# Performance work log

Hardware: AMD Instinct MI355X
Metric: run time of the kernel (lower is better)

The kernel has to match this reference:

```python
import jax, jax.numpy as jnp
import numpy as np

B, N, D, H = 2, 64, 256, 8
DK = D // H
EPS = 1e-5


def layer_norm(x, g, b):
    mu = jnp.mean(x, axis=-1, keepdims=True)
    var = jnp.var(x, axis=-1, keepdims=True)
    return (x - mu) * jax.lax.rsqrt(var + EPS) * g + b


def setup_inputs() -> dict:
    key = jax.random.key(0)
    ks = jax.random.split(key, 12)
    s = 1.0 / np.sqrt(D)
    inp = {
        "x": jax.random.normal(ks[0], (B, N, N, D), jnp.float32),
        "W_lk": jax.random.uniform(ks[1], (D, D), jnp.float32, -s, s),
        "W_rk": jax.random.uniform(ks[2], (D, D), jnp.float32, -s, s),
        "W_lv": jax.random.uniform(ks[3], (D, D), jnp.float32, -s, s),
        "W_rv": jax.random.uniform(ks[4], (D, D), jnp.float32, -s, s),
        "W_out": jax.random.uniform(ks[5], (D, D), jnp.float32, -s, s),
        "ln_agg_g": jnp.ones((D,), jnp.float32),
        "ln_agg_b": jnp.zeros((D,), jnp.float32),
        "W1": jax.random.uniform(ks[6], (D, 2 * D), jnp.float32, -s, s),
        "b1": jnp.zeros((2 * D,), jnp.float32),
        "W2": jax.random.uniform(ks[7], (2 * D, D), jnp.float32, -1.0 / np.sqrt(2 * D), 1.0 / np.sqrt(2 * D)),
        "b2": jnp.zeros((D,), jnp.float32),
        "ln2_g": jnp.ones((D,), jnp.float32),
        "ln2_b": jnp.zeros((D,), jnp.float32),
    }
    return inp


def reference(x, W_lk, W_rk, W_lv, W_rv, W_out, ln_agg_g, ln_agg_b, W1, b1, W2, b2, ln2_g, ln2_b):
    b, n = x.shape[0], x.shape[1]
    # projections (no bias), split into heads: [b, n, n, H, DK]
    lk = (x @ W_lk).reshape(b, n, n, H, DK)
    rk = (x @ W_rk).reshape(b, n, n, H, DK)
    lv = (x @ W_lv).reshape(b, n, n, H, DK)
    rv = (x @ W_rv).reshape(b, n, n, H, DK)
    # triangle attention scores over intermediate node 'a'
    scores = jnp.einsum('bxahd,bayhd->bxayh', lk, rk) / np.sqrt(DK)
    att = jax.nn.softmax(scores, axis=2)
    # fused triangle value aggregation: sum_a att * lv[x,a] * rv[a,y]
    o = jnp.einsum('bxayh,bxahd,bayhd->bxyhd', att, lv, rv)
    o = o.reshape(b, n, n, D) @ W_out
    # FFN block (dropout = 0)
    h = layer_norm(x + o, ln_agg_g, ln_agg_b)
    m = jax.nn.relu(h @ W1 + b1) @ W2 + b2
    return layer_norm(m + h, ln2_g, ln2_b)
```

## Files before the change

kernel.cpp:

```cpp
#include <hip/hip_runtime.h>

#define ROWS 8192
#define DIM  256

typedef short short8 __attribute__((ext_vector_type(8)));
typedef float f4     __attribute__((ext_vector_type(4)));

__device__ __forceinline__ float bf2f(unsigned int u16) {
    union { unsigned int i; float f; } v;
    v.i = (u16 & 0xffffu) << 16;
    return v.f;
}
__device__ __forceinline__ unsigned short f2bf(float f) {
    union { float f; unsigned int u; } v; v.f = f;
    unsigned int r = v.u + 0x7fffu + ((v.u >> 16) & 1u);
    return (unsigned short)(r >> 16);
}

__global__ __launch_bounds__(256)
void cast_all(const float* __restrict__ x, unsigned short* __restrict__ xb,
              const float* __restrict__ w0, const float* __restrict__ w1,
              const float* __restrict__ w2, const float* __restrict__ w3,
              const float* __restrict__ w4, const float* __restrict__ w5,
              const float* __restrict__ w6, unsigned short* __restrict__ wt)
{
    if (blockIdx.x < 2048) {
        const size_t i = ((size_t)blockIdx.x * 256 + threadIdx.x) * 4;
        float4 v = *(const float4*)(x + i);
        uint2 p;
        p.x = f2bf(v.x) | ((unsigned int)f2bf(v.y) << 16);
        p.y = f2bf(v.z) | ((unsigned int)f2bf(v.w) << 16);
        *(uint2*)(xb + i) = p;
        return;
    }
    __shared__ float t[32][33];
    int id = blockIdx.x - 2048;
    const float* src; int K, N, Ntiles; size_t doff;
    if (id < 320) {
        int w = id >> 6; id &= 63; K = 256; N = 256; Ntiles = 8;
        doff = (size_t)w * 65536;
        src = (w == 0) ? w0 : (w == 1) ? w1 : (w == 2) ? w2 : (w == 3) ? w3 : w4;
    } else if (id < 448) {
        id -= 320; K = 256; N = 512; Ntiles = 16; doff = 327680; src = w5;
    } else {
        id -= 448; K = 512; N = 256; Ntiles = 8;  doff = 458752; src = w6;
    }
    const int tk = id / Ntiles, tn = id % Ntiles;
    const int k0 = tk * 32, n0 = tn * 32;
    const int c = threadIdx.x & 31, r8 = threadIdx.x >> 5;
    for (int rr = r8; rr < 32; rr += 8)
        t[rr][c] = src[(size_t)(k0 + rr) * N + n0 + c];
    __syncthreads();
    for (int rr = r8; rr < 32; rr += 8)
        wt[doff + (size_t)(n0 + rr) * K + k0 + c] = f2bf(t[c][rr]);
}

__global__ __launch_bounds__(1024, 1)
void proj_mfma(const unsigned short* __restrict__ A, const unsigned short* __restrict__ WT,
               unsigned short* __restrict__ projT)
{
    __shared__ unsigned short WL[256 * 256];
    const int lane = threadIdx.x & 63, wave = threadIdx.x >> 6;
    const int wsel = blockIdx.x;
    const int col0 = (wave >> 2) * 64;
    const int m0 = blockIdx.y * 128 + (wave & 3) * 32;
    const int lm = lane & 15, lk8 = (lane >> 4) * 8;
    const unsigned short* W = WT + (size_t)wsel * 65536;
    unsigned short* dst = projT + (size_t)wsel * 2097152;

    {
        const int tid = threadIdx.x;
        #pragma unroll
        for (int it = 0; it < 8; ++it) {
            const int c = tid + it * 1024;
            const int col = c >> 5, ch = c & 31;
            const uint4 v = *(const uint4*)(W + (size_t)col * 256 + ch * 8);
            *(uint4*)((char*)WL + col * 512 + ((ch ^ (col & 7)) << 4)) = v;
        }
    }
    __syncthreads();

    f4 acc[2][4];
    #pragma unroll
    for (int i = 0; i < 2; ++i)
        #pragma unroll
        for (int j = 0; j < 4; ++j) acc[i][j] = (f4){0.f, 0.f, 0.f, 0.f};

    #pragma unroll 2
    for (int kc = 0; kc < 256; kc += 32) {
        short8 af[2], bf[4];
        #pragma unroll
        for (int i = 0; i < 2; ++i)
            af[i] = *(const short8*)(A + (size_t)(m0 + i * 16 + lm) * 256 + kc + lk8);
        #pragma unroll
        for (int j = 0; j < 4; ++j) {
            const int cl = col0 + j * 16 + lm;
            const int kch = (kc + lk8) >> 3;
            bf[j] = *(const short8*)((char*)WL + cl * 512 + ((kch ^ (cl & 7)) << 4));
        }
        #pragma unroll
        for (int i = 0; i < 2; ++i)
            #pragma unroll
            for (int j = 0; j < 4; ++j)
                acc[i][j] = __builtin_amdgcn_mfma_f32_16x16x32_bf16(af[i], bf[j], acc[i][j], 0, 0, 0);
    }

    const int rbase = (lane >> 4) * 4;
    const int swap = (wsel == 3);
    #pragma unroll
    for (int i = 0; i < 2; ++i)
        #pragma unroll
        for (int j = 0; j < 4; ++j) {
            const int c = col0 + j * 16 + lm;
            const int h = c >> 5, d = c & 31;
            #pragma unroll
            for (int r = 0; r < 4; ++r) {
                const int m = m0 + i * 16 + rbase + r;
                const int b = m >> 12, ii = (m >> 6) & 63, jj = m & 63;
                const int p = swap ? jj : ii;
                const int q = swap ? ii : jj;
                const size_t idx = ((((size_t)b * 8 + h) * 64 + p) * 64 + q) * 32 + d;
                dst[idx] = f2bf(acc[i][j][r]);
            }
        }
}

__global__ __launch_bounds__(256)
void scores_mfma(const unsigned short* __restrict__ lkT, const unsigned short* __restrict__ rkT,
                 unsigned short* __restrict__ S)
{
    const int lane = threadIdx.x & 63, wave = threadIdx.x >> 6;
    const int bi = blockIdx.x;
    const int b = bi >> 7, h = (bi >> 4) & 7, a = (bi & 15) * 4 + wave;
    const size_t bh = (size_t)b * 8 + h;
    const int lm = lane & 15, lk8 = (lane >> 4) * 8;

    short8 af[4], bf[4];
    #pragma unroll
    for (int t = 0; t < 4; ++t) {
        af[t] = *(const short8*)(lkT + ((bh * 64 + (t * 16 + lm)) * 64 + a) * 32 + lk8);
        bf[t] = *(const short8*)(rkT + ((bh * 64 + a) * 64 + (t * 16 + lm)) * 32 + lk8);
    }
    const int rbase = (lane >> 4) * 4;
    unsigned short* Sb = S + bh * 262144 + a * 64;
    #pragma unroll
    for (int mt = 0; mt < 4; ++mt)
        #pragma unroll
        for (int nt = 0; nt < 4; ++nt) {
            f4 acc = (f4){0.f, 0.f, 0.f, 0.f};
            acc = __builtin_amdgcn_mfma_f32_16x16x32_bf16(af[mt], bf[nt], acc, 0, 0, 0);
            #pragma unroll
            for (int r = 0; r < 4; ++r) {
                const int xx = mt * 16 + rbase + r;
                const int yy = nt * 16 + lm;
                Sb[(size_t)xx * 4096 + yy] = f2bf(acc[r] * 0.17677669529663687f);
            }
        }
}

__global__ __launch_bounds__(256)
void softmax_agg(const unsigned short* __restrict__ S, const unsigned short* __restrict__ lvT,
                 const unsigned short* __restrict__ rvT, unsigned short* __restrict__ obuf)
{
    __shared__ float att[64][64];
    __shared__ float lvL[64][32];
    __shared__ float smx[4][64], ssm[4][64], invL[64];
    const int bi = blockIdx.x;
    const int b = bi >> 9, h = (bi >> 6) & 7, x = bi & 63;
    const size_t bh = (size_t)b * 8 + h;
    const int tid = threadIdx.x;

    {
        const int a = tid >> 2, yo = (tid & 3) * 16;
        const unsigned short* Sp = S + (bh * 64 + x) * 4096 + a * 64 + yo;
        uint4 p0 = *(const uint4*)(Sp);
        uint4 p1 = *(const uint4*)(Sp + 8);
        att[a][yo +  0] = bf2f(p0.x); att[a][yo +  1] = bf2f(p0.x >> 16);
        att[a][yo +  2] = bf2f(p0.y); att[a][yo +  3] = bf2f(p0.y >> 16);
        att[a][yo +  4] = bf2f(p0.z); att[a][yo +  5] = bf2f(p0.z >> 16);
        att[a][yo +  6] = bf2f(p0.w); att[a][yo +  7] = bf2f(p0.w >> 16);
        att[a][yo +  8] = bf2f(p1.x); att[a][yo +  9] = bf2f(p1.x >> 16);
        att[a][yo + 10] = bf2f(p1.y); att[a][yo + 11] = bf2f(p1.y >> 16);
        att[a][yo + 12] = bf2f(p1.z); att[a][yo + 13] = bf2f(p1.z >> 16);
        att[a][yo + 14] = bf2f(p1.w); att[a][yo + 15] = bf2f(p1.w >> 16);
        const int d0 = (tid & 3) * 8;
        uint4 q = *(const uint4*)(lvT + ((bh * 64 + x) * 64 + a) * 32 + d0);
        lvL[a][d0 + 0] = bf2f(q.x); lvL[a][d0 + 1] = bf2f(q.x >> 16);
        lvL[a][d0 + 2] = bf2f(q.y); lvL[a][d0 + 3] = bf2f(q.y >> 16);
        lvL[a][d0 + 4] = bf2f(q.z); lvL[a][d0 + 5] = bf2f(q.z >> 16);
        lvL[a][d0 + 6] = bf2f(q.w); lvL[a][d0 + 7] = bf2f(q.w >> 16);
    }
    __syncthreads();

    {
        const int y = tid & 63, az = tid >> 6;
        float mx = -1e30f;
        for (int a = az; a < 64; a += 4) mx = fmaxf(mx, att[a][y]);
        smx[az][y] = mx;
    }
    __syncthreads();

    {
        const int y = tid & 63, az = tid >> 6;
        const float mx = fmaxf(fmaxf(smx[0][y], smx[1][y]), fmaxf(smx[2][y], smx[3][y]));
        float s = 0.f;
        for (int a = az; a < 64; a += 4) {
            float e = __expf(att[a][y] - mx);
            att[a][y] = e;
            s += e;
        }
        ssm[az][y] = s;
    }
    __syncthreads();
    if (tid < 64)
        invL[tid] = 1.f / (ssm[0][tid] + ssm[1][tid] + ssm[2][tid] + ssm[3][tid]);
    __syncthreads();

    {
        const int dp = tid & 15, yb = tid >> 4;
        #pragma unroll
        for (int it = 0; it < 4; ++it) {
            const int y = yb + it * 16;
            const unsigned short* rvr = rvT + (bh * 64 + y) * 2048 + dp * 2;
            float a0 = 0.f, a1 = 0.f;
            #pragma unroll 8
            for (int a = 0; a < 64; ++a) {
                unsigned int pk = *(const unsigned int*)(rvr + a * 32);
                float w = att[a][y];
                a0 = fmaf(w * lvL[a][2 * dp],     bf2f(pk),       a0);
                a1 = fmaf(w * lvL[a][2 * dp + 1], bf2f(pk >> 16), a1);
            }
            const float inv = invL[y];
            a0 *= inv; a1 *= inv;
            unsigned int st = f2bf(a0) | ((unsigned int)f2bf(a1) << 16);
            *(unsigned int*)(obuf + (((size_t)b * 64 + x) * 64 + y) * 256 + h * 32 + dp * 2) = st;
        }
    }
}

__device__ __forceinline__ int swz8(int r, int c, int rl) {
    return r * rl + ((((c >> 3) ^ (r & 7)) << 3) | (c & 7));
}

__global__ __launch_bounds__(512, 2)
void ffn_fused(const unsigned short* __restrict__ A,
               const unsigned short* __restrict__ WoT,
               const unsigned short* __restrict__ W1T,
               const unsigned short* __restrict__ W2T,
               const float* __restrict__ xres,
               const float* __restrict__ g1, const float* __restrict__ be1,
               const float* __restrict__ b1, const float* __restrict__ b2,
               const float* __restrict__ g2, const float* __restrict__ be2,
               float* __restrict__ out)
{
    __shared__ unsigned short hs[32 * 256];
    __shared__ unsigned short ms[32 * 512];
    __shared__ float ps[32][8], pq[32][8];
    const int lane = threadIdx.x & 63, wave = threadIdx.x >> 6;
    const int m0 = blockIdx.x * 32;
    const int lm = lane & 15, lk8 = (lane >> 4) * 8;
    const int rbase = (lane >> 4) * 4;
    const int col0 = wave * 32;
    const int rot8  = (blockIdx.x >> 3) & 7;
    const int rot16 = (blockIdx.x >> 3) & 15;
    float hreg[2][2][4];

    {
        f4 acc[2][2];
        #pragma unroll
        for (int i = 0; i < 2; ++i)
            #pragma unroll
            for (int j = 0; j < 2; ++j) acc[i][j] = (f4){0.f, 0.f, 0.f, 0.f};
        #pragma unroll
        for (int t = 0; t < 8; ++t) {
            const int kc = ((t + rot8) & 7) * 32;
            short8 af[2], bf[2];
            #pragma unroll
            for (int i = 0; i < 2; ++i)
                af[i] = *(const short8*)(A + (size_t)(m0 + i * 16 + lm) * 256 + kc + lk8);
            #pragma unroll
            for (int j = 0; j < 2; ++j)
                bf[j] = *(const short8*)(WoT + (size_t)(col0 + j * 16 + lm) * 256 + kc + lk8);
            #pragma unroll
            for (int i = 0; i < 2; ++i)
                #pragma unroll
                for (int j = 0; j < 2; ++j)
                    acc[i][j] = __builtin_amdgcn_mfma_f32_16x16x32_bf16(af[i], bf[j], acc[i][j], 0, 0, 0);
        }
        float v[2][2][4], s[2][4], q[2][4];
        #pragma unroll
        for (int i = 0; i < 2; ++i)
            #pragma unroll
            for (int r = 0; r < 4; ++r) { s[i][r] = 0.f; q[i][r] = 0.f; }
        #pragma unroll
        for (int i = 0; i < 2; ++i)
            #pragma unroll
            for (int j = 0; j < 2; ++j) {
                const int n = col0 + j * 16 + lm;
                #pragma unroll
                for (int r = 0; r < 4; ++r) {
                    const float t = acc[i][j][r] + xres[(size_t)(m0 + i * 16 + rbase + r) * 256 + n];
                    v[i][j][r] = t;
                    s[i][r] += t;
                    q[i][r] = fmaf(t, t, q[i][r]);
                }
            }
        #pragma unroll
        for (int off = 1; off < 16; off <<= 1)
            #pragma unroll
            for (int i = 0; i < 2; ++i)
                #pragma unroll
                for (int r = 0; r < 4; ++r) {
                    s[i][r] += __shfl_xor(s[i][r], off);
                    q[i][r] += __shfl_xor(q[i][r], off);
                }
        if (lm == 0)
            #pragma unroll
            for (int i = 0; i < 2; ++i)
                #pragma unroll
                for (int r = 0; r < 4; ++r) {
                    ps[i * 16 + rbase + r][wave] = s[i][r];
                    pq[i * 16 + rbase + r][wave] = q[i][r];
                }
        __syncthreads();
        #pragma unroll
        for (int i = 0; i < 2; ++i)
            #pragma unroll
            for (int r = 0; r < 4; ++r) {
                const int lr = i * 16 + rbase + r;
                const float Sm = ps[lr][0] + ps[lr][1] + ps[lr][2] + ps[lr][3]
                               + ps[lr][4] + ps[lr][5] + ps[lr][6] + ps[lr][7];
                const float Qm = pq[lr][0] + pq[lr][1] + pq[lr][2] + pq[lr][3]
                               + pq[lr][4] + pq[lr][5] + pq[lr][6] + pq[lr][7];
                const float mu = Sm * (1.f / 256.f);
                const float ri = rsqrtf(Qm * (1.f / 256.f) - mu * mu + 1e-5f);
                #pragma unroll
                for (int j = 0; j < 2; ++j) {
                    const int n = col0 + j * 16 + lm;
                    const unsigned short hb16 = f2bf((v[i][j][r] - mu) * ri * g1[n] + be1[n]);
                    hs[swz8(lr, n, 256)] = hb16;
                    hreg[i][j][r] = bf2f(hb16);
                }
            }
    }
    __syncthreads();

    {
        const int c0 = wave * 64;
        f4 acc2[2][4];
        #pragma unroll
        for (int i = 0; i < 2; ++i)
            #pragma unroll
            for (int j = 0; j < 4; ++j) acc2[i][j] = (f4){0.f, 0.f, 0.f, 0.f};
        #pragma unroll
        for (int t = 0; t < 8; ++t) {
            const int kc = ((t + rot8) & 7) * 32;
            short8 af[2], bf[4];
            #pragma unroll
            for (int i = 0; i < 2; ++i)
                af[i] = *(const short8*)(hs + swz8(i * 16 + lm, kc + lk8, 256));
            #pragma unroll
            for (int j = 0; j < 4; ++j)
                bf[j] = *(const short8*)(W1T + (size_t)(c0 + j * 16 + lm) * 256 + kc + lk8);
            #pragma unroll
            for (int i = 0; i < 2; ++i)
                #pragma unroll
                for (int j = 0; j < 4; ++j)
                    acc2[i][j] = __builtin_amdgcn_mfma_f32_16x16x32_bf16(af[i], bf[j], acc2[i][j], 0, 0, 0);
        }
        #pragma unroll
        for (int i = 0; i < 2; ++i)
            #pragma unroll
            for (int j = 0; j < 4; ++j) {
                const int n = c0 + j * 16 + lm;
                const float bb = b1[n];
                #pragma unroll
                for (int r = 0; r < 4; ++r)
                    ms[swz8(i * 16 + rbase + r, n, 512)] = f2bf(fmaxf(acc2[i][j][r] + bb, 0.f));
            }
    }
    __syncthreads();

    {
        f4 acc[2][2];
        #pragma unroll
        for (int i = 0; i < 2; ++i)
            #pragma unroll
            for (int j = 0; j < 2; ++j) acc[i][j] = (f4){0.f, 0.f, 0.f, 0.f};
        #pragma unroll
        for (int t = 0; t < 16; ++t) {
            const int kc = ((t + rot16) & 15) * 32;
            short8 af[2], bf[2];
            #pragma unroll
            for (int i = 0; i < 2; ++i)
                af[i] = *(const short8*)(ms + swz8(i * 16 + lm, kc + lk8, 512));
            #pragma unroll
            for (int j = 0; j < 2; ++j)
                bf[j] = *(const short8*)(W2T + (size_t)(col0 + j * 16 + lm) * 512 + kc + lk8);
            #pragma unroll
            for (int i = 0; i < 2; ++i)
                #pragma unroll
                for (int j = 0; j < 2; ++j)
                    acc[i][j] = __builtin_amdgcn_mfma_f32_16x16x32_bf16(af[i], bf[j], acc[i][j], 0, 0, 0);
        }
        float v[2][2][4], s[2][4], q[2][4];
        #pragma unroll
        for (int i = 0; i < 2; ++i)
            #pragma unroll
            for (int r = 0; r < 4; ++r) { s[i][r] = 0.f; q[i][r] = 0.f; }
        #pragma unroll
        for (int i = 0; i < 2; ++i)
            #pragma unroll
            for (int j = 0; j < 2; ++j) {
                const int n = col0 + j * 16 + lm;
                const float bb = b2[n];
                #pragma unroll
                for (int r = 0; r < 4; ++r) {
                    const float t = acc[i][j][r] + bb + hreg[i][j][r];
                    v[i][j][r] = t;
                    s[i][r] += t;
                    q[i][r] = fmaf(t, t, q[i][r]);
                }
            }
        #pragma unroll
        for (int off = 1; off < 16; off <<= 1)
            #pragma unroll
            for (int i = 0; i < 2; ++i)
                #pragma unroll
                for (int r = 0; r < 4; ++r) {
                    s[i][r] += __shfl_xor(s[i][r], off);
                    q[i][r] += __shfl_xor(q[i][r], off);
                }
        if (lm == 0)
            #pragma unroll
            for (int i = 0; i < 2; ++i)
                #pragma unroll
                for (int r = 0; r < 4; ++r) {
                    ps[i * 16 + rbase + r][wave] = s[i][r];
                    pq[i * 16 + rbase + r][wave] = q[i][r];
                }
        __syncthreads();
        #pragma unroll
        for (int i = 0; i < 2; ++i)
            #pragma unroll
            for (int r = 0; r < 4; ++r) {
                const int lr = i * 16 + rbase + r;
                const float Sm = ps[lr][0] + ps[lr][1] + ps[lr][2] + ps[lr][3]
                               + ps[lr][4] + ps[lr][5] + ps[lr][6] + ps[lr][7];
                const float Qm = pq[lr][0] + pq[lr][1] + pq[lr][2] + pq[lr][3]
                               + pq[lr][4] + pq[lr][5] + pq[lr][6] + pq[lr][7];
                const float mu = Sm * (1.f / 256.f);
                const float ri = rsqrtf(Qm * (1.f / 256.f) - mu * mu + 1e-5f);
                const int m = m0 + lr;
                #pragma unroll
                for (int j = 0; j < 2; ++j) {
                    const int n = col0 + j * 16 + lm;
                    out[(size_t)m * 256 + n] = (v[i][j][r] - mu) * ri * g2[n] + be2[n];
                }
            }
    }
}

extern "C" void kernel_launch(void* const* d_in, const int* in_sizes, int n_in,
                              void* d_out, int out_size, void* d_ws, size_t ws_size,
                              hipStream_t stream)
{
    const float* x    = (const float*)d_in[0];
    const float* Wlk  = (const float*)d_in[1];
    const float* Wrk  = (const float*)d_in[2];
    const float* Wlv  = (const float*)d_in[3];
    const float* Wrv  = (const float*)d_in[4];
    const float* Wout = (const float*)d_in[5];
    const float* g1   = (const float*)d_in[6];
    const float* be1  = (const float*)d_in[7];
    const float* W1   = (const float*)d_in[8];
    const float* b1   = (const float*)d_in[9];
    const float* W2   = (const float*)d_in[10];
    const float* b2   = (const float*)d_in[11];
    const float* g2   = (const float*)d_in[12];
    const float* be2  = (const float*)d_in[13];

    char* base = (char*)d_ws;
    const size_t MB = 1ull << 20;
    unsigned short* xb    = (unsigned short*)(base + 0);
    unsigned short* obufb = (unsigned short*)(base + 0);
    unsigned short* projT = (unsigned short*)(base + 4 * MB);
    unsigned short* lkT   = projT;
    unsigned short* rkT   = projT + 2097152;
    unsigned short* lvT   = projT + 2 * 2097152;
    unsigned short* rvT   = projT + 3 * 2097152;
    unsigned short* Sbuf  = (unsigned short*)(base + 32 * MB);
    unsigned short* WT    = (unsigned short*)(base + 40 * MB);

    cast_all<<<2624, 256, 0, stream>>>(x, xb, Wlk, Wrk, Wlv, Wrv, Wout, W1, W2, WT);
    proj_mfma<<<dim3(4, 64), 1024, 0, stream>>>(xb, WT, projT);
    scores_mfma<<<256, 256, 0, stream>>>(lkT, rkT, Sbuf);
    softmax_agg<<<1024, 256, 0, stream>>>(Sbuf, lvT, rvT, obufb);
    ffn_fused<<<256, 512, 0, stream>>>(obufb, WT + 262144, WT + 327680, WT + 458752,
                                       x, g1, be1, b1, b2, g2, be2, (float*)d_out);
}
```

Before: 158.2 us.

## Stage FFN weights through double-buffered LDS via async global_load_lds

The fused FFN kernel now loads each K-slice of WoT, W1T and W2T into a double-buffered shared-memory buffer with global_load_lds, prefetching the next slice while MFMAs run on the current one. The A tile is also staged into LDS, and residual values are preloaded into registers. This replaces direct per-wave global loads of the weight fragments with shared, asynchronous staging. In exchange it adds about 80KB of LDS per block, which may reduce occupancy below the launch bound of 2 blocks, adds a barrier every K step, and removes the per-block K rotation.

```diff
diff --git a/kernel.cpp b/kernel.cpp
--- a/kernel.cpp
+++ b/kernel.cpp
@@ -16,6 +16,10 @@
     unsigned int r = v.u + 0x7fffu + ((v.u >> 16) & 1u);
     return (unsigned short)(r >> 16);
 }
+
+#define GLD(g, l) __builtin_amdgcn_global_load_lds( \
+    (const __attribute__((address_space(1))) void*)(g), \
+    (__attribute__((address_space(3))) void*)(l), 16, 0, 0)
 
 __global__ __launch_bounds__(256)
 void cast_all(const float* __restrict__ x, unsigned short* __restrict__ xb,
@@ -253,74 +257,109 @@
                const float* __restrict__ g2, const float* __restrict__ be2,
                float* __restrict__ out)
 {
+    __shared__ unsigned short As[32 * 256];
     __shared__ unsigned short hs[32 * 256];
     __shared__ unsigned short ms[32 * 512];
+    __shared__ unsigned short wbuf[2 * 16384];
     __shared__ float ps[32][8], pq[32][8];
     const int lane = threadIdx.x & 63, wave = threadIdx.x >> 6;
     const int m0 = blockIdx.x * 32;
     const int lm = lane & 15, lk8 = (lane >> 4) * 8;
-    const int rbase = (lane >> 4) * 4;
+    const int og = lane >> 4;
+    const int rbase = og * 4;
     const int col0 = wave * 32;
-    const int rot8  = (blockIdx.x >> 3) & 7;
-    const int rot16 = (blockIdx.x >> 3) & 15;
     float hreg[2][2][4];
 
+    float xr[2][2][4];
+    #pragma unroll
+    for (int i = 0; i < 2; ++i)
+        #pragma unroll
+        for (int j = 0; j < 2; ++j)
+            #pragma unroll
+            for (int r = 0; r < 4; ++r)
+                xr[i][j][r] = xres[(size_t)(m0 + i * 16 + rbase + r) * 256 + col0 + j * 16 + lm];
+
+    #pragma unroll
+    for (int s = 0; s < 2; ++s) {
+        const int idx = (wave * 2 + s) * 64 + lane;
+        GLD(A + (size_t)(m0 + (idx & 31)) * 256 + (idx >> 5) * 8, As + (wave * 2 + s) * 512);
+    }
+    #pragma unroll
+    for (int s = 0; s < 2; ++s) {
+        const int idx = (wave * 2 + s) * 64 + lane;
+        GLD(WoT + (size_t)(idx & 255) * 256 + (idx >> 8) * 8, wbuf + (wave * 2 + s) * 512);
+    }
+    __syncthreads();
+
     {
         f4 acc[2][2];
         #pragma unroll
         for (int i = 0; i < 2; ++i)
             #pragma unroll
             for (int j = 0; j < 2; ++j) acc[i][j] = (f4){0.f, 0.f, 0.f, 0.f};
-        #pragma unroll
         for (int t = 0; t < 8; ++t) {
-            const int kc = ((t + rot8) & 7) * 32;
+            if (t < 7) {
+                unsigned short* db = wbuf + ((t + 1) & 1) * 8192;
+                const int kcn = (t + 1) * 32;
+                #pragma unroll
+                for (int s = 0; s < 2; ++s) {
+                    const int idx = (wave * 2 + s) * 64 + lane;
+                    GLD(WoT + (size_t)(idx & 255) * 256 + kcn + (idx >> 8) * 8, db + (wave * 2 + s) * 512);
+                }
+            }
+            const unsigned short* wb = wbuf + (t & 1) * 8192;
+            const int oA = t * 4 + og;
             short8 af[2], bf[2];
             #pragma unroll
             for (int i = 0; i < 2; ++i)
-                af[i] = *(const short8*)(A + (size_t)(m0 + i * 16 + lm) * 256 + kc + lk8);
+                af[i] = *(const short8*)(As + (oA * 32 + i * 16 + lm) * 8);
             #pragma unroll
             for (int j = 0; j < 2; ++j)
-                bf[j] = *(const short8*)(WoT + (size_t)(col0 + j * 16 + lm) * 256 + kc + lk8);
+                bf[j] = *(const short8*)(wb + (og * 256 + col0 + j * 16 + lm) * 8);
             #pragma unroll
             for (int i = 0; i < 2; ++i)
                 #pragma unroll
                 for (int j = 0; j < 2; ++j)
                     acc[i][j] = __builtin_amdgcn_mfma_f32_16x16x32_bf16(af[i], bf[j], acc[i][j], 0, 0, 0);
-        }
-        float v[2][2][4], s[2][4], q[2][4];
-        #pragma unroll
-        for (int i = 0; i < 2; ++i)
-            #pragma unroll
-            for (int r = 0; r < 4; ++r) { s[i][r] = 0.f; q[i][r] = 0.f; }
-        #pragma unroll
-        for (int i = 0; i < 2; ++i)
-            #pragma unroll
-            for (int j = 0; j < 2; ++j) {
-                const int n = col0 + j * 16 + lm;
+            __syncthreads();
+        }
+        #pragma unroll
+        for (int s = 0; s < 4; ++s) {
+            const int idx = (wave * 4 + s) * 64 + lane;
+            GLD(W1T + (size_t)(idx & 511) * 256 + (idx >> 9) * 8, wbuf + (wave * 4 + s) * 512);
+        }
+        float v[2][2][4], s1[2][4], q1[2][4];
+        #pragma unroll
+        for (int i = 0; i < 2; ++i)
+            #pragma unroll
+            for (int r = 0; r < 4; ++r) { s1[i][r] = 0.f; q1[i][r] = 0.f; }
+        #pragma unroll
+        for (int i = 0; i < 2; ++i)
+            #pragma unroll
+            for (int j = 0; j < 2; ++j)
                 #pragma unroll
                 for (int r = 0; r < 4; ++r) {
-                    const float t = acc[i][j][r] + xres[(size_t)(m0 + i * 16 + rbase + r) * 256 + n];
+                    const float t = acc[i][j][r] + xr[i][j][r];
                     v[i][j][r] = t;
-                    s[i][r] += t;
-                    q[i][r] = fmaf(t, t, q[i][r]);
-                }
-            }
+                    s1[i][r] += t;
+                    q1[i][r] = fmaf(t, t, q1[i][r]);
+                }
         #pragma unroll
         for (int off = 1; off < 16; off <<= 1)
             #pragma unroll
             for (int i = 0; i < 2; ++i)
                 #pragma unroll
                 for (int r = 0; r < 4; ++r) {
-                    s[i][r] += __shfl_xor(s[i][r], off);
-                    q[i][r] += __shfl_xor(q[i][r], off);
+                    s1[i][r] += __shfl_xor(s1[i][r], off);
+                    q1[i][r] += __shfl_xor(q1[i][r], off);
                 }
         if (lm == 0)
             #pragma unroll
             for (int i = 0; i < 2; ++i)
                 #pragma unroll
                 for (int r = 0; r < 4; ++r) {
-                    ps[i * 16 + rbase + r][wave] = s[i][r];
-                    pq[i * 16 + rbase + r][wave] = q[i][r];
+                    ps[i * 16 + rbase + r][wave] = s1[i][r];
+                    pq[i * 16 + rbase + r][wave] = q1[i][r];
                 }
         __syncthreads();
         #pragma unroll
@@ -352,21 +391,36 @@
         for (int i = 0; i < 2; ++i)
             #pragma unroll
             for (int j = 0; j < 4; ++j) acc2[i][j] = (f4){0.f, 0.f, 0.f, 0.f};
-        #pragma unroll
         for (int t = 0; t < 8; ++t) {
-            const int kc = ((t + rot8) & 7) * 32;
+            if (t < 7) {
+                unsigned short* db = wbuf + ((t + 1) & 1) * 16384;
+                const int kcn = (t + 1) * 32;
+                #pragma unroll
+                for (int s = 0; s < 4; ++s) {
+                    const int idx = (wave * 4 + s) * 64 + lane;
+                    GLD(W1T + (size_t)(idx & 511) * 256 + kcn + (idx >> 9) * 8, db + (wave * 4 + s) * 512);
+                }
+            }
+            const unsigned short* wb = wbuf + (t & 1) * 16384;
+            const int kc = t * 32;
             short8 af[2], bf[4];
             #pragma unroll
             for (int i = 0; i < 2; ++i)
                 af[i] = *(const short8*)(hs + swz8(i * 16 + lm, kc + lk8, 256));
             #pragma unroll
             for (int j = 0; j < 4; ++j)
-                bf[j] = *(const short8*)(W1T + (size_t)(c0 + j * 16 + lm) * 256 + kc + lk8);
+                bf[j] = *(const short8*)(wb + (og * 512 + c0 + j * 16 + lm) * 8);
             #pragma unroll
             for (int i = 0; i < 2; ++i)
                 #pragma unroll
                 for (int j = 0; j < 4; ++j)
                     acc2[i][j] = __builtin_amdgcn_mfma_f32_16x16x32_bf16(af[i], bf[j], acc2[i][j], 0, 0, 0);
+            __syncthreads();
+        }
+        #pragma unroll
+        for (int s = 0; s < 2; ++s) {
+            const int idx = (wave * 2 + s) * 64 + lane;
+            GLD(W2T + (size_t)(idx & 255) * 512 + (idx >> 8) * 8, wbuf + (wave * 2 + s) * 512);
         }
         #pragma unroll
         for (int i = 0; i < 2; ++i)
@@ -387,27 +441,37 @@
         for (int i = 0; i < 2; ++i)
             #pragma unroll
             for (int j = 0; j < 2; ++j) acc[i][j] = (f4){0.f, 0.f, 0.f, 0.f};
-        #pragma unroll
         for (int t = 0; t < 16; ++t) {
-            const int kc = ((t + rot16) & 15) * 32;
+            if (t < 15) {
+                unsigned short* db = wbuf + ((t + 1) & 1) * 8192;
+                const int kcn = (t + 1) * 32;
+                #pragma unroll
+                for (int s = 0; s < 2; ++s) {
+                    const int idx = (wave * 2 + s) * 64 + lane;
+                    GLD(W2T + (size_t)(idx & 255) * 512 + kcn + (idx >> 8) * 8, db + (wave * 2 + s) * 512);
+                }
+            }
+            const unsigned short* wb = wbuf + (t & 1) * 8192;
+            const int kc = t * 32;
             short8 af[2], bf[2];
             #pragma unroll
             for (int i = 0; i < 2; ++i)
                 af[i] = *(const short8*)(ms + swz8(i * 16 + lm, kc + lk8, 512));
             #pragma unroll
             for (int j = 0; j < 2; ++j)
-                bf[j] = *(const short8*)(W2T + (size_t)(col0 + j * 16 + lm) * 512 + kc + lk8);
+                bf[j] = *(const short8*)(wb + (og * 256 + col0 + j * 16 + lm) * 8);
             #pragma unroll
             for (int i = 0; i < 2; ++i)
                 #pragma unroll
                 for (int j = 0; j < 2; ++j)
                     acc[i][j] = __builtin_amdgcn_mfma_f32_16x16x32_bf16(af[i], bf[j], acc[i][j], 0, 0, 0);
-        }
-        float v[2][2][4], s[2][4], q[2][4];
-        #pragma unroll
-        for (int i = 0; i < 2; ++i)
-            #pragma unroll
-            for (int r = 0; r < 4; ++r) { s[i][r] = 0.f; q[i][r] = 0.f; }
+            __syncthreads();
+        }
+        float v[2][2][4], s3[2][4], q3[2][4];
+        #pragma unroll
+        for (int i = 0; i < 2; ++i)
+            #pragma unroll
+            for (int r = 0; r < 4; ++r) { s3[i][r] = 0.f; q3[i][r] = 0.f; }
         #pragma unroll
         for (int i = 0; i < 2; ++i)
             #pragma unroll
@@ -418,8 +482,8 @@
                 for (int r = 0; r < 4; ++r) {
                     const float t = acc[i][j][r] + bb + hreg[i][j][r];
                     v[i][j][r] = t;
-                    s[i][r] += t;
-                    q[i][r] = fmaf(t, t, q[i][r]);
+                    s3[i][r] += t;
+                    q3[i][r] = fmaf(t, t, q3[i][r]);
                 }
             }
         #pragma unroll
@@ -428,16 +492,16 @@
             for (int i = 0; i < 2; ++i)
                 #pragma unroll
                 for (int r = 0; r < 4; ++r) {
-                    s[i][r] += __shfl_xor(s[i][r], off);
-                    q[i][r] += __shfl_xor(q[i][r], off);
+                    s3[i][r] += __shfl_xor(s3[i][r], off);
+                    q3[i][r] += __shfl_xor(q3[i][r], off);
                 }
         if (lm == 0)
             #pragma unroll
             for (int i = 0; i < 2; ++i)
                 #pragma unroll
                 for (int r = 0; r < 4; ++r) {
-                    ps[i * 16 + rbase + r][wave] = s[i][r];
-                    pq[i * 16 + rbase + r][wave] = q[i][r];
+                    ps[i * 16 + rbase + r][wave] = s3[i][r];
+                    pq[i * 16 + rbase + r][wave] = q3[i][r];
                 }
         __syncthreads();
         #pragma unroll
```

Result: slower. 165.2 us (+4.4%).
